# Optimization experiments

Hardware: AMD Instinct MI355X
Metric: run time of the kernel (lower is better)

The kernel has to match this reference:

```python
import jax, jax.numpy as jnp
import numpy as np

T, D, E, I = 2048, 2048, 16, 1408  # tokens, hidden, experts, moe intermediate


def setup_inputs() -> dict:
    key = jax.random.key(0)
    k1, k2, k3, k4 = jax.random.split(key, 4)
    return {
        "hidden_states": jax.random.normal(k1, (T, D), dtype=jnp.float32),
        "gate_w": jax.random.normal(k2, (E, D), dtype=jnp.float32) * 0.02,
        "w13": jax.random.normal(k3, (E, 2 * I, D), dtype=jnp.float32) * 0.02,
        "w2": jax.random.normal(k4, (E, D, I), dtype=jnp.float32) * 0.02,
        "top_k": 6,
    }


def reference(hidden_states, gate_w, w13, w2, top_k):
    x = hidden_states                               # [T, D]
    n_tokens, n_experts = x.shape[0], gate_w.shape[0]

    # Router gate + softmax + top-k (select_experts, use_grouped_topk=False)
    router_logits = x @ gate_w.T                    # [T, E]
    probs = jax.nn.softmax(router_logits, axis=-1)
    topk_w, topk_ids = jax.lax.top_k(probs, top_k)  # [T, K]
    # renormalize=True
    topk_w = topk_w / jnp.sum(topk_w, axis=-1, keepdims=True)

    # Dense combine weights [T, E]: scatter top-k weights to their experts
    combine = jnp.zeros((n_tokens, n_experts), dtype=x.dtype)
    combine = combine.at[jnp.arange(n_tokens)[:, None], topk_ids].add(topk_w)

    # Fused MoE experts: SwiGLU (w13 = fused gate+up), activation='silu'
    w1g = w13[:, : w13.shape[1] // 2, :]            # [E, I, D] gate proj
    w1u = w13[:, w13.shape[1] // 2 :, :]            # [E, I, D] up proj
    g = jnp.einsum("td,eid->tei", x, w1g)           # [T, E, I]
    u = jnp.einsum("td,eid->tei", x, w1u)
    h = jax.nn.silu(g) * u                          # [T, E, I]
    # Down proj + weighted combine over experts
    out = jnp.einsum("tei,edi,te->td", h, w2, combine)  # [T, D]
    return out
```

## Files before the change

### kernel.cpp

```cpp
#include <hip/hip_runtime.h>

#define T_TOK 2048
#define DIM 2048
#define NE 16
#define NI 1408
#define TOPK 6

typedef __bf16 bf16x8 __attribute__((ext_vector_type(8)));
typedef float f32x4 __attribute__((ext_vector_type(4)));

static __device__ __forceinline__ unsigned short f2bf(float f) {
  unsigned int u = __builtin_bit_cast(unsigned int, f);
  u += 0x7fffu + ((u >> 16) & 1u);
  return (unsigned short)(u >> 16);
}

static __device__ __forceinline__ void async_load16(const void* g, void* l) {
  __builtin_amdgcn_global_load_lds(
      (const __attribute__((address_space(1))) unsigned int*)g,
      (__attribute__((address_space(3))) unsigned int*)l, 16, 0, 0);
}

__global__ void router_kernel(const float* __restrict__ x, const float* __restrict__ gw,
                              float* __restrict__ combine) {
  int t = blockIdx.x;
  int l = threadIdx.x;
  const float* xr = x + (size_t)t * DIM;
  float acc[NE];
#pragma unroll
  for (int e = 0; e < NE; e++) acc[e] = 0.f;
  for (int d = l; d < DIM; d += 64) {
    float xv = xr[d];
#pragma unroll
    for (int e = 0; e < NE; e++) acc[e] += xv * gw[e * DIM + d];
  }
#pragma unroll
  for (int e = 0; e < NE; e++) {
    float v = acc[e];
#pragma unroll
    for (int s = 32; s > 0; s >>= 1) v += __shfl_down(v, s, 64);
    acc[e] = v;
  }
  if (l == 0) {
    float mx = acc[0];
#pragma unroll
    for (int e = 1; e < NE; e++) mx = fmaxf(mx, acc[e]);
    float p[NE]; float sum = 0.f;
#pragma unroll
    for (int e = 0; e < NE; e++) { p[e] = expf(acc[e] - mx); sum += p[e]; }
    float inv = 1.f / sum;
#pragma unroll
    for (int e = 0; e < NE; e++) p[e] *= inv;
    float w[NE];
#pragma unroll
    for (int e = 0; e < NE; e++) w[e] = 0.f;
    int used = 0;
    float ssum = 0.f;
    for (int k = 0; k < TOPK; k++) {
      int best = 0; float bv = -1e30f;
      for (int e = 0; e < NE; e++) {
        if (!((used >> e) & 1) && acc[e] > bv) { bv = acc[e]; best = e; }
      }
      used |= (1 << best);
      w[best] = p[best];
      ssum += p[best];
    }
    float isum = 1.f / ssum;
    for (int e = 0; e < NE; e++) combine[t * NE + e] = w[e] * isum;
  }
}

__global__ void cast_x_kernel(const float* __restrict__ x, unsigned short* __restrict__ xb) {
  int i = (blockIdx.x * 256 + threadIdx.x) * 4;
  float4 v = *(const float4*)(x + i);
  ushort4 o = make_ushort4(f2bf(v.x), f2bf(v.y), f2bf(v.z), f2bf(v.w));
  *(ushort4*)(xb + i) = o;
}

__global__ void count_kernel(const float* __restrict__ combine, int* __restrict__ counts) {
  int e = blockIdx.x, l = threadIdx.x;
  int c = 0;
  for (int t0 = 0; t0 < T_TOK; t0 += 64) {
    bool pred = combine[(size_t)(t0 + l) * NE + e] > 0.f;
    unsigned long long m = __ballot(pred);
    c += (int)__popcll(m);
  }
  if (l == 0) counts[e] = c;
}

__global__ void scan_kernel(const int* __restrict__ counts, int* __restrict__ offsets) {
  if (threadIdx.x == 0) {
    int s = 0;
    for (int e = 0; e < NE; e++) { offsets[e] = s; s += counts[e]; }
    offsets[NE] = s;
  }
}

__global__ void fill_kernel(const float* __restrict__ combine, const int* __restrict__ offsets,
                            int* __restrict__ ids, float* __restrict__ scales) {
  int e = blockIdx.x, l = threadIdx.x;
  int base = offsets[e];
  for (int t0 = 0; t0 < T_TOK; t0 += 64) {
    int t = t0 + l;
    float w = combine[(size_t)t * NE + e];
    bool pred = w > 0.f;
    unsigned long long m = __ballot(pred);
    int idx = base + (int)__popcll(m & ((1ull << l) - 1ull));
    if (pred) { ids[idx] = t; scales[idx] = w; }
    base += (int)__popcll(m);
  }
}

__global__ __launch_bounds__(256) void gemm1_kernel(
    const unsigned short* __restrict__ xb, const float* __restrict__ w13,
    const int* __restrict__ ids, const int* __restrict__ offsets,
    unsigned short* __restrict__ h) {
  int e = blockIdx.z;
  int off = offsets[e];
  int ne = offsets[e + 1] - off;
  int m0 = blockIdx.y * 128;
  if (m0 >= ne) return;
  int i0 = blockIdx.x * 64;

  __shared__ unsigned short At[8 * 128 * 8];
  __shared__ unsigned short Bg[8 * 64 * 8];
  __shared__ unsigned short Bu[8 * 64 * 8];
  __shared__ int ids_l[128];

  int tid = threadIdx.x;
  int wave = tid >> 6, lane = tid & 63;

  if (tid < 128) {
    int s = m0 + tid;
    ids_l[tid] = (s < ne) ? ids[off + s] : 0;
  }
  __syncthreads();
  int gid0 = ids_l[lane];
  int gid1 = ids_l[64 + lane];
  const unsigned short* a0 = xb + (size_t)gid0 * DIM;
  const unsigned short* a1 = xb + (size_t)gid1 * DIM;

  const float* We = w13 + (size_t)e * (2 * NI) * DIM;
  const float* Wg = We + (size_t)i0 * DIM;
  const float* Wu = We + (size_t)(NI + i0) * DIM;

  int wm = wave >> 1, wn = wave & 1;
  int quad = lane >> 4, l15 = lane & 15;

  f32x4 zf = {0.f, 0.f, 0.f, 0.f};
  f32x4 accg[4][2], accu[4][2];
#pragma unroll
  for (int a = 0; a < 4; a++)
#pragma unroll
    for (int b = 0; b < 2; b++) { accg[a][b] = zf; accu[a][b] = zf; }

  int brow = tid >> 4;
  int c4 = tid & 15;
  int bchunk = c4 >> 1;
  int hof = (c4 & 1) * 4;

  for (int k0 = 0; k0 < DIM; k0 += 64) {
#pragma unroll
    for (int j = 0; j < 4; j++) {
      int linear = wave * 4 + j;
      int chunk = linear >> 1;
      int half = j & 1;
      const unsigned short* src = (half ? a1 : a0) + k0 + chunk * 8;
      async_load16(src, &At[chunk * 1024 + half * 512]);
    }
#pragma unroll
    for (int r = 0; r < 4; r++) {
      int row = brow + r * 16;
      float4 vg = *(const float4*)(Wg + (size_t)row * DIM + k0 + c4 * 4);
      float4 vu = *(const float4*)(Wu + (size_t)row * DIM + k0 + c4 * 4);
      ushort4 og = make_ushort4(f2bf(vg.x), f2bf(vg.y), f2bf(vg.z), f2bf(vg.w));
      ushort4 ou = make_ushort4(f2bf(vu.x), f2bf(vu.y), f2bf(vu.z), f2bf(vu.w));
      *(ushort4*)&Bg[bchunk * 512 + row * 8 + hof] = og;
      *(ushort4*)&Bu[bchunk * 512 + row * 8 + hof] = ou;
    }
    __syncthreads();
#pragma unroll
    for (int ks = 0; ks < 2; ks++) {
      int cb = ks * 4 + quad;
      bf16x8 af[4], bgf[2], buf_[2];
#pragma unroll
      for (int mt = 0; mt < 4; mt++)
        af[mt] = *(const bf16x8*)&At[cb * 1024 + (wm * 64 + mt * 16 + l15) * 8];
#pragma unroll
      for (int nt = 0; nt < 2; nt++) {
        bgf[nt] = *(const bf16x8*)&Bg[cb * 512 + (wn * 32 + nt * 16 + l15) * 8];
        buf_[nt] = *(const bf16x8*)&Bu[cb * 512 + (wn * 32 + nt * 16 + l15) * 8];
      }
#pragma unroll
      for (int mt = 0; mt < 4; mt++)
#pragma unroll
        for (int nt = 0; nt < 2; nt++) {
          accg[mt][nt] = __builtin_amdgcn_mfma_f32_16x16x32_bf16(af[mt], bgf[nt], accg[mt][nt], 0, 0, 0);
          accu[mt][nt] = __builtin_amdgcn_mfma_f32_16x16x32_bf16(af[mt], buf_[nt], accu[mt][nt], 0, 0, 0);
        }
    }
    __syncthreads();
  }
#pragma unroll
  for (int mt = 0; mt < 4; mt++)
#pragma unroll
    for (int nt = 0; nt < 2; nt++)
#pragma unroll
      for (int r = 0; r < 4; r++) {
        int row_l = wm * 64 + mt * 16 + quad * 4 + r;
        if (m0 + row_l < ne) {
          float gv = accg[mt][nt][r];
          float uv = accu[mt][nt][r];
          float hv = gv * uv / (1.f + __expf(-gv));
          int col = i0 + wn * 32 + nt * 16 + l15;
          h[(size_t)(off + m0 + row_l) * NI + col] = f2bf(hv);
        }
      }
}

__global__ __launch_bounds__(256) void gemm2_kernel(
    const unsigned short* __restrict__ h, const float* __restrict__ w2,
    const int* __restrict__ ids, const float* __restrict__ scales,
    const int* __restrict__ offsets, float* __restrict__ out) {
  int e = blockIdx.z;
  int off = offsets[e];
  int ne = offsets[e + 1] - off;
  int m0 = blockIdx.y * 128;
  if (m0 >= ne) return;
  int n0 = blockIdx.x * 128;

  __shared__ unsigned short At[8 * 128 * 8];
  __shared__ unsigned short Bt[8 * 128 * 8];
  __shared__ int ids_l[128];
  __shared__ float scl_l[128];

  int tid = threadIdx.x;
  int wave = tid >> 6, lane = tid & 63;
  if (tid < 128) {
    int s = m0 + tid;
    bool v = s < ne;
    ids_l[tid] = v ? ids[off + s] : 0;
    scl_l[tid] = v ? scales[off + s] : 0.f;
  }
  __syncthreads();

  const unsigned short* h0 = h + (size_t)(off + m0 + lane) * NI;
  const unsigned short* h1 = h + (size_t)(off + m0 + 64 + lane) * NI;
  const float* W = w2 + (size_t)e * DIM * NI;

  int wm = wave >> 1, wn = wave & 1;
  int quad = lane >> 4, l15 = lane & 15;

  f32x4 zf = {0.f, 0.f, 0.f, 0.f};
  f32x4 acc[4][4];
#pragma unroll
  for (int a = 0; a < 4; a++)
#pragma unroll
    for (int b = 0; b < 4; b++) acc[a][b] = zf;

  int brow = tid >> 4, c4 = tid & 15, bchunk = c4 >> 1, hof = (c4 & 1) * 4;

  for (int k0 = 0; k0 < NI; k0 += 64) {
#pragma unroll
    for (int j = 0; j < 4; j++) {
      int linear = wave * 4 + j;
      int chunk = linear >> 1;
      int half = j & 1;
      const unsigned short* src = (half ? h1 : h0) + k0 + chunk * 8;
      async_load16(src, &At[chunk * 1024 + half * 512]);
    }
#pragma unroll
    for (int r = 0; r < 8; r++) {
      int row = brow + r * 16;
      float4 v = *(const float4*)(W + (size_t)(n0 + row) * NI + k0 + c4 * 4);
      ushort4 o = make_ushort4(f2bf(v.x), f2bf(v.y), f2bf(v.z), f2bf(v.w));
      *(ushort4*)&Bt[bchunk * 1024 + row * 8 + hof] = o;
    }
    __syncthreads();
#pragma unroll
    for (int ks = 0; ks < 2; ks++) {
      int cb = ks * 4 + quad;
      bf16x8 af[4], bf[4];
#pragma unroll
      for (int mt = 0; mt < 4; mt++)
        af[mt] = *(const bf16x8*)&At[cb * 1024 + (wm * 64 + mt * 16 + l15) * 8];
#pragma unroll
      for (int nt = 0; nt < 4; nt++)
        bf[nt] = *(const bf16x8*)&Bt[cb * 1024 + (wn * 64 + nt * 16 + l15) * 8];
#pragma unroll
      for (int mt = 0; mt < 4; mt++)
#pragma unroll
        for (int nt = 0; nt < 4; nt++)
          acc[mt][nt] = __builtin_amdgcn_mfma_f32_16x16x32_bf16(af[mt], bf[nt], acc[mt][nt], 0, 0, 0);
    }
    __syncthreads();
  }
#pragma unroll
  for (int mt = 0; mt < 4; mt++)
#pragma unroll
    for (int nt = 0; nt < 4; nt++)
#pragma unroll
      for (int r = 0; r < 4; r++) {
        int row_l = wm * 64 + mt * 16 + quad * 4 + r;
        if (m0 + row_l < ne) {
          int t = ids_l[row_l];
          float s = scl_l[row_l];
          int col = n0 + wn * 64 + nt * 16 + l15;
          atomicAdd(&out[(size_t)t * DIM + col], s * acc[mt][nt][r]);
        }
      }
}

extern "C" void kernel_launch(void* const* d_in, const int* in_sizes, int n_in,
                              void* d_out, int out_size, void* d_ws, size_t ws_size,
                              hipStream_t stream) {
  const float* x   = (const float*)d_in[0];
  const float* gw  = (const float*)d_in[1];
  const float* w13 = (const float*)d_in[2];
  const float* w2  = (const float*)d_in[3];
  float* out = (float*)d_out;

  char* ws = (char*)d_ws;
  float* combine        = (float*)(ws + 0x000000);
  int* counts           = (int*)  (ws + 0x020000);
  int* offsets          = (int*)  (ws + 0x020100);
  int* ids              = (int*)  (ws + 0x020200);
  float* scales         = (float*)(ws + 0x02D000);
  unsigned short* xb    = (unsigned short*)(ws + 0x040000);
  unsigned short* h     = (unsigned short*)(ws + 0x840000);

  hipMemsetAsync(d_out, 0, (size_t)T_TOK * DIM * sizeof(float), stream);

  router_kernel<<<T_TOK, 64, 0, stream>>>(x, gw, combine);
  cast_x_kernel<<<(T_TOK * DIM) / (256 * 4), 256, 0, stream>>>(x, xb);
  count_kernel<<<NE, 64, 0, stream>>>(combine, counts);
  scan_kernel<<<1, 64, 0, stream>>>(counts, offsets);
  fill_kernel<<<NE, 64, 0, stream>>>(combine, offsets, ids, scales);

  gemm1_kernel<<<dim3(NI / 64, T_TOK / 128, NE), 256, 0, stream>>>(xb, w13, ids, offsets, h);
  gemm2_kernel<<<dim3(DIM / 128, T_TOK / 128, NE), 256, 0, stream>>>(h, w2, ids, scales, offsets, out);
}
```

Measured before the change: 1.201 ms.

## Pre-cast expert weights to bf16 in chunks before grouped GEMMs

Adds a weight-cast kernel that converts chunks of w13 and w2 from fp32 to bf16 in workspace, then runs new GEMM kernels that load bf16 weights directly with async LDS loads. The old kernels re-read fp32 weights and converted them in each tile, so the same weights were fetched and converted once per token block. The new path adds an extra full pass over the weights and more kernel launches per chunk. It needs enough workspace, and falls back to the old kernels when there is not enough.

```diff
diff --git a/kernel.cpp b/kernel.cpp
--- a/kernel.cpp
+++ b/kernel.cpp
@@ -75,6 +75,16 @@
   float4 v = *(const float4*)(x + i);
   ushort4 o = make_ushort4(f2bf(v.x), f2bf(v.y), f2bf(v.z), f2bf(v.w));
   *(ushort4*)(xb + i) = o;
+}
+
+__global__ void cast_w_kernel(const float* __restrict__ src, unsigned short* __restrict__ dst,
+                              int n4) {
+  int stride = gridDim.x * 256;
+  for (int i = blockIdx.x * 256 + threadIdx.x; i < n4; i += stride) {
+    float4 v = ((const float4*)src)[i];
+    ushort4 o = make_ushort4(f2bf(v.x), f2bf(v.y), f2bf(v.z), f2bf(v.w));
+    ((ushort4*)dst)[i] = o;
+  }
 }
 
 __global__ void count_kernel(const float* __restrict__ combine, int* __restrict__ counts) {
@@ -111,7 +121,188 @@
   }
 }
 
-__global__ __launch_bounds__(256) void gemm1_kernel(
+
+__global__ __launch_bounds__(256) void gemm1_pre_kernel(
+    const unsigned short* __restrict__ xb, const unsigned short* __restrict__ wb,
+    const int* __restrict__ ids, const int* __restrict__ offsets,
+    unsigned short* __restrict__ h, int e_base) {
+  int ez = blockIdx.z;
+  int e = e_base + ez;
+  int off = offsets[e];
+  int ne = offsets[e + 1] - off;
+  int m0 = blockIdx.y * 128;
+  if (m0 >= ne) return;
+  int i0 = blockIdx.x * 64;
+
+  __shared__ unsigned short At[8 * 128 * 8];
+  __shared__ unsigned short Bg[8 * 64 * 8];
+  __shared__ unsigned short Bu[8 * 64 * 8];
+  __shared__ int ids_l[128];
+
+  int tid = threadIdx.x;
+  int wave = tid >> 6, lane = tid & 63;
+
+  if (tid < 128) {
+    int s = m0 + tid;
+    ids_l[tid] = (s < ne) ? ids[off + s] : 0;
+  }
+  __syncthreads();
+  const unsigned short* a0 = xb + (size_t)ids_l[lane] * DIM;
+  const unsigned short* a1 = xb + (size_t)ids_l[64 + lane] * DIM;
+  const unsigned short* wg = wb + ((size_t)ez * (2 * NI) + i0 + lane) * DIM;
+  const unsigned short* wu = wb + ((size_t)ez * (2 * NI) + NI + i0 + lane) * DIM;
+
+  int wm = wave >> 1, wn = wave & 1;
+  int quad = lane >> 4, l15 = lane & 15;
+
+  f32x4 zf = {0.f, 0.f, 0.f, 0.f};
+  f32x4 accg[4][2], accu[4][2];
+#pragma unroll
+  for (int a = 0; a < 4; a++)
+#pragma unroll
+    for (int b = 0; b < 2; b++) { accg[a][b] = zf; accu[a][b] = zf; }
+
+  for (int k0 = 0; k0 < DIM; k0 += 64) {
+#pragma unroll
+    for (int j = 0; j < 4; j++) {
+      int linear = wave * 4 + j;
+      int c = linear >> 1;
+      int half = j & 1;
+      async_load16((half ? a1 : a0) + k0 + c * 8, &At[c * 1024 + half * 512]);
+    }
+#pragma unroll
+    for (int j = 0; j < 2; j++) {
+      int c = wave * 2 + j;
+      async_load16(wg + k0 + c * 8, &Bg[c * 512]);
+      async_load16(wu + k0 + c * 8, &Bu[c * 512]);
+    }
+    __syncthreads();
+#pragma unroll
+    for (int ks = 0; ks < 2; ks++) {
+      int cb = ks * 4 + quad;
+      bf16x8 af[4], bgf[2], buf_[2];
+#pragma unroll
+      for (int mt = 0; mt < 4; mt++)
+        af[mt] = *(const bf16x8*)&At[cb * 1024 + (wm * 64 + mt * 16 + l15) * 8];
+#pragma unroll
+      for (int nt = 0; nt < 2; nt++) {
+        bgf[nt] = *(const bf16x8*)&Bg[cb * 512 + (wn * 32 + nt * 16 + l15) * 8];
+        buf_[nt] = *(const bf16x8*)&Bu[cb * 512 + (wn * 32 + nt * 16 + l15) * 8];
+      }
+#pragma unroll
+      for (int mt = 0; mt < 4; mt++)
+#pragma unroll
+        for (int nt = 0; nt < 2; nt++) {
+          accg[mt][nt] = __builtin_amdgcn_mfma_f32_16x16x32_bf16(af[mt], bgf[nt], accg[mt][nt], 0, 0, 0);
+          accu[mt][nt] = __builtin_amdgcn_mfma_f32_16x16x32_bf16(af[mt], buf_[nt], accu[mt][nt], 0, 0, 0);
+        }
+    }
+    __syncthreads();
+  }
+#pragma unroll
+  for (int mt = 0; mt < 4; mt++)
+#pragma unroll
+    for (int nt = 0; nt < 2; nt++)
+#pragma unroll
+      for (int r = 0; r < 4; r++) {
+        int row_l = wm * 64 + mt * 16 + quad * 4 + r;
+        if (m0 + row_l < ne) {
+          float gv = accg[mt][nt][r];
+          float uv = accu[mt][nt][r];
+          float hv = gv * uv / (1.f + __expf(-gv));
+          int col = i0 + wn * 32 + nt * 16 + l15;
+          h[(size_t)(off + m0 + row_l) * NI + col] = f2bf(hv);
+        }
+      }
+}
+
+__global__ __launch_bounds__(256) void gemm2_pre_kernel(
+    const unsigned short* __restrict__ h, const unsigned short* __restrict__ wb,
+    const int* __restrict__ ids, const float* __restrict__ scales,
+    const int* __restrict__ offsets, float* __restrict__ out, int e_base) {
+  int ez = blockIdx.z;
+  int e = e_base + ez;
+  int off = offsets[e];
+  int ne = offsets[e + 1] - off;
+  int m0 = blockIdx.y * 128;
+  if (m0 >= ne) return;
+  int n0 = blockIdx.x * 128;
+
+  __shared__ unsigned short At[8 * 128 * 8];
+  __shared__ unsigned short Bt[8 * 128 * 8];
+  __shared__ int ids_l[128];
+  __shared__ float scl_l[128];
+
+  int tid = threadIdx.x;
+  int wave = tid >> 6, lane = tid & 63;
+  if (tid < 128) {
+    int s = m0 + tid;
+    bool v = s < ne;
+    ids_l[tid] = v ? ids[off + s] : 0;
+    scl_l[tid] = v ? scales[off + s] : 0.f;
+  }
+  __syncthreads();
+
+  const unsigned short* h0 = h + (size_t)(off + m0 + lane) * NI;
+  const unsigned short* h1 = h + (size_t)(off + m0 + 64 + lane) * NI;
+  const unsigned short* b0 = wb + ((size_t)ez * DIM + n0 + lane) * NI;
+  const unsigned short* b1 = b0 + (size_t)64 * NI;
+
+  int wm = wave >> 1, wn = wave & 1;
+  int quad = lane >> 4, l15 = lane & 15;
+
+  f32x4 zf = {0.f, 0.f, 0.f, 0.f};
+  f32x4 acc[4][4];
+#pragma unroll
+  for (int a = 0; a < 4; a++)
+#pragma unroll
+    for (int b = 0; b < 4; b++) acc[a][b] = zf;
+
+  for (int k0 = 0; k0 < NI; k0 += 64) {
+#pragma unroll
+    for (int j = 0; j < 4; j++) {
+      int linear = wave * 4 + j;
+      int c = linear >> 1;
+      int half = j & 1;
+      async_load16((half ? h1 : h0) + k0 + c * 8, &At[c * 1024 + half * 512]);
+      async_load16((half ? b1 : b0) + k0 + c * 8, &Bt[c * 1024 + half * 512]);
+    }
+    __syncthreads();
+#pragma unroll
+    for (int ks = 0; ks < 2; ks++) {
+      int cb = ks * 4 + quad;
+      bf16x8 af[4], bf[4];
+#pragma unroll
+      for (int mt = 0; mt < 4; mt++)
+        af[mt] = *(const bf16x8*)&At[cb * 1024 + (wm * 64 + mt * 16 + l15) * 8];
+#pragma unroll
+      for (int nt = 0; nt < 4; nt++)
+        bf[nt] = *(const bf16x8*)&Bt[cb * 1024 + (wn * 64 + nt * 16 + l15) * 8];
+#pragma unroll
+      for (int mt = 0; mt < 4; mt++)
+#pragma unroll
+        for (int nt = 0; nt < 4; nt++)
+          acc[mt][nt] = __builtin_amdgcn_mfma_f32_16x16x32_bf16(af[mt], bf[nt], acc[mt][nt], 0, 0, 0);
+    }
+    __syncthreads();
+  }
+#pragma unroll
+  for (int mt = 0; mt < 4; mt++)
+#pragma unroll
+    for (int nt = 0; nt < 4; nt++)
+#pragma unroll
+      for (int r = 0; r < 4; r++) {
+        int row_l = wm * 64 + mt * 16 + quad * 4 + r;
+        if (m0 + row_l < ne) {
+          int t = ids_l[row_l];
+          float s = scl_l[row_l];
+          int col = n0 + wn * 64 + nt * 16 + l15;
+          atomicAdd(&out[(size_t)t * DIM + col], s * acc[mt][nt][r]);
+        }
+      }
+}
+
+__global__ __launch_bounds__(256) void gemm1_fb_kernel(
     const unsigned short* __restrict__ xb, const float* __restrict__ w13,
     const int* __restrict__ ids, const int* __restrict__ offsets,
     unsigned short* __restrict__ h) {
@@ -218,7 +409,7 @@
       }
 }
 
-__global__ __launch_bounds__(256) void gemm2_kernel(
+__global__ __launch_bounds__(256) void gemm2_fb_kernel(
     const unsigned short* __restrict__ h, const float* __restrict__ w2,
     const int* __restrict__ ids, const float* __restrict__ scales,
     const int* __restrict__ offsets, float* __restrict__ out) {
@@ -328,6 +519,14 @@
   float* scales         = (float*)(ws + 0x02D000);
   unsigned short* xb    = (unsigned short*)(ws + 0x040000);
   unsigned short* h     = (unsigned short*)(ws + 0x840000);
+  unsigned short* wb    = (unsigned short*)(ws + 0x2A00000);
+
+  const size_t wb_off = 0x2A00000;
+  const size_t per_e13 = (size_t)(2 * NI) * DIM * 2;
+  int chunk = 0;
+  if      (ws_size >= wb_off + 8 * per_e13) chunk = 8;
+  else if (ws_size >= wb_off + 4 * per_e13) chunk = 4;
+  else if (ws_size >= wb_off + 2 * per_e13) chunk = 2;
 
   hipMemsetAsync(d_out, 0, (size_t)T_TOK * DIM * sizeof(float), stream);
 
@@ -337,6 +536,21 @@
   scan_kernel<<<1, 64, 0, stream>>>(counts, offsets);
   fill_kernel<<<NE, 64, 0, stream>>>(combine, offsets, ids, scales);
 
-  gemm1_kernel<<<dim3(NI / 64, T_TOK / 128, NE), 256, 0, stream>>>(xb, w13, ids, offsets, h);
-  gemm2_kernel<<<dim3(DIM / 128, T_TOK / 128, NE), 256, 0, stream>>>(h, w2, ids, scales, offsets, out);
-}
+  if (chunk) {
+    for (int b = 0; b < NE; b += chunk) {
+      int n4 = chunk * 2 * NI * DIM / 4;
+      cast_w_kernel<<<2048, 256, 0, stream>>>(w13 + (size_t)b * (2 * NI) * DIM, wb, n4);
+      gemm1_pre_kernel<<<dim3(NI / 64, T_TOK / 128, chunk), 256, 0, stream>>>(
+          xb, wb, ids, offsets, h, b);
+    }
+    for (int b = 0; b < NE; b += chunk) {
+      int n4 = chunk * DIM * NI / 4;
+      cast_w_kernel<<<2048, 256, 0, stream>>>(w2 + (size_t)b * DIM * NI, wb, n4);
+      gemm2_pre_kernel<<<dim3(DIM / 128, T_TOK / 128, chunk), 256, 0, stream>>>(
+          h, wb, ids, scales, offsets, out, b);
+    }
+  } else {
+    gemm1_fb_kernel<<<dim3(NI / 64, T_TOK / 128, NE), 256, 0, stream>>>(xb, w13, ids, offsets, h);
+    gemm2_fb_kernel<<<dim3(DIM / 128, T_TOK / 128, NE), 256, 0, stream>>>(h, w2, ids, scales, offsets, out);
+  }
+}
```

New measurement: 1.326 ms. +10.5%, slower.

## Double-buffer LDS tiles, swizzle B layout, and remap grid for XCD locality

Applied to the files above, without the earlier changes.

Both expert GEMM kernels now double-buffer the A and B shared-memory tiles. The next tile's async A loads and global B loads are issued before the current tile's MFMAs, which drops one barrier per k-step and overlaps memory with compute. The B tile is written with an XOR swizzle to reduce LDS bank conflicts, and the 3D grid is flattened into a 1D grid with an interleaved block-to-tile mapping across the 8 XCDs. In exchange, shared memory per block doubles and register pressure rises from holding prefetched B values, which may lower occupancy.

```diff
diff --git a/kernel.cpp b/kernel.cpp
--- a/kernel.cpp
+++ b/kernel.cpp
@@ -115,16 +115,21 @@
     const unsigned short* __restrict__ xb, const float* __restrict__ w13,
     const int* __restrict__ ids, const int* __restrict__ offsets,
     unsigned short* __restrict__ h) {
-  int e = blockIdx.z;
+  int bid = blockIdx.x;
+  int lin = (bid & 7) * (5632 >> 3) + (bid >> 3);
+  int iy = lin & 15;
+  int ix = (lin >> 4) % 22;
+  int e  = lin / 352;
+
   int off = offsets[e];
   int ne = offsets[e + 1] - off;
-  int m0 = blockIdx.y * 128;
+  int m0 = iy * 128;
   if (m0 >= ne) return;
-  int i0 = blockIdx.x * 64;
-
-  __shared__ unsigned short At[8 * 128 * 8];
-  __shared__ unsigned short Bg[8 * 64 * 8];
-  __shared__ unsigned short Bu[8 * 64 * 8];
+  int i0 = ix * 64;
+
+  __shared__ unsigned short At[2][8 * 128 * 8];
+  __shared__ unsigned short Bg[2][8 * 64 * 8];
+  __shared__ unsigned short Bu[2][8 * 64 * 8];
   __shared__ int ids_l[128];
 
   int tid = threadIdx.x;
@@ -135,10 +140,8 @@
     ids_l[tid] = (s < ne) ? ids[off + s] : 0;
   }
   __syncthreads();
-  int gid0 = ids_l[lane];
-  int gid1 = ids_l[64 + lane];
-  const unsigned short* a0 = xb + (size_t)gid0 * DIM;
-  const unsigned short* a1 = xb + (size_t)gid1 * DIM;
+  const unsigned short* a0 = xb + (size_t)ids_l[lane] * DIM;
+  const unsigned short* a1 = xb + (size_t)ids_l[64 + lane] * DIM;
 
   const float* We = w13 + (size_t)e * (2 * NI) * DIM;
   const float* Wg = We + (size_t)i0 * DIM;
@@ -147,60 +150,85 @@
   int wm = wave >> 1, wn = wave & 1;
   int quad = lane >> 4, l15 = lane & 15;
 
-  f32x4 zf = {0.f, 0.f, 0.f, 0.f};
-  f32x4 accg[4][2], accu[4][2];
-#pragma unroll
-  for (int a = 0; a < 4; a++)
-#pragma unroll
-    for (int b = 0; b < 2; b++) { accg[a][b] = zf; accu[a][b] = zf; }
-
   int brow = tid >> 4;
   int c4 = tid & 15;
   int bchunk = c4 >> 1;
-  int hof = (c4 & 1) * 4;
-
-  for (int k0 = 0; k0 < DIM; k0 += 64) {
-#pragma unroll
-    for (int j = 0; j < 4; j++) {
-      int linear = wave * 4 + j;
-      int chunk = linear >> 1;
-      int half = j & 1;
-      const unsigned short* src = (half ? a1 : a0) + k0 + chunk * 8;
-      async_load16(src, &At[chunk * 1024 + half * 512]);
-    }
-#pragma unroll
-    for (int r = 0; r < 4; r++) {
-      int row = brow + r * 16;
-      float4 vg = *(const float4*)(Wg + (size_t)row * DIM + k0 + c4 * 4);
-      float4 vu = *(const float4*)(Wu + (size_t)row * DIM + k0 + c4 * 4);
-      ushort4 og = make_ushort4(f2bf(vg.x), f2bf(vg.y), f2bf(vg.z), f2bf(vg.w));
-      ushort4 ou = make_ushort4(f2bf(vu.x), f2bf(vu.y), f2bf(vu.z), f2bf(vu.w));
-      *(ushort4*)&Bg[bchunk * 512 + row * 8 + hof] = og;
-      *(ushort4*)&Bu[bchunk * 512 + row * 8 + hof] = ou;
-    }
+  int hof2 = (c4 & 1) * 8;
+
+  f32x4 zf = {0.f, 0.f, 0.f, 0.f};
+  f32x4 accg[4][2], accu[4][2];
+#pragma unroll
+  for (int a = 0; a < 4; a++)
+#pragma unroll
+    for (int b = 0; b < 2; b++) { accg[a][b] = zf; accu[a][b] = zf; }
+
+#define G1_STAGE_A(P, K0)                                                      \
+  _Pragma("unroll") for (int j = 0; j < 4; j++) {                              \
+    int c = (wave * 4 + j) >> 1;                                               \
+    int half = j & 1;                                                          \
+    async_load16((half ? a1 : a0) + (K0) + c * 8, &At[P][c * 1024 + half * 512]); \
+  }
+
+#define G1_LOAD_B(K0)                                                          \
+  _Pragma("unroll") for (int r = 0; r < 4; r++) {                              \
+    int row = brow + r * 16;                                                   \
+    vg[r] = *(const float4*)(Wg + (size_t)row * DIM + (K0) + c4 * 4);          \
+    vu[r] = *(const float4*)(Wu + (size_t)row * DIM + (K0) + c4 * 4);          \
+  }
+
+#define G1_WRITE_B(P)                                                          \
+  _Pragma("unroll") for (int r = 0; r < 4; r++) {                              \
+    int row = brow + r * 16;                                                   \
+    int swz = (bchunk * 1024 + row * 16 + hof2) ^ (bchunk << 4);               \
+    ushort4 og = make_ushort4(f2bf(vg[r].x), f2bf(vg[r].y), f2bf(vg[r].z), f2bf(vg[r].w)); \
+    ushort4 ou = make_ushort4(f2bf(vu[r].x), f2bf(vu[r].y), f2bf(vu[r].z), f2bf(vu[r].w)); \
+    *(ushort4*)((char*)&Bg[P][0] + swz) = og;                                  \
+    *(ushort4*)((char*)&Bu[P][0] + swz) = ou;                                  \
+  }
+
+#define G1_COMPUTE(P)                                                          \
+  _Pragma("unroll") for (int ks = 0; ks < 2; ks++) {                           \
+    int cb = ks * 4 + quad;                                                    \
+    int cbx = cb << 4;                                                         \
+    bf16x8 af[4], bgf[2], buf_[2];                                             \
+    const char* Ab = (const char*)&At[P][0];                                   \
+    const char* Bgb = (const char*)&Bg[P][0];                                  \
+    const char* Bub = (const char*)&Bu[P][0];                                  \
+    _Pragma("unroll") for (int mt = 0; mt < 4; mt++)                           \
+      af[mt] = *(const bf16x8*)(Ab + cb * 2048 + (wm * 64 + mt * 16 + l15) * 16); \
+    _Pragma("unroll") for (int nt = 0; nt < 2; nt++) {                         \
+      int rb = cb * 1024 + (wn * 32 + nt * 16 + l15) * 16;                     \
+      bgf[nt] = *(const bf16x8*)(Bgb + (rb ^ cbx));                            \
+      buf_[nt] = *(const bf16x8*)(Bub + (rb ^ cbx));                           \
+    }                                                                          \
+    _Pragma("unroll") for (int mt = 0; mt < 4; mt++)                           \
+      _Pragma("unroll") for (int nt = 0; nt < 2; nt++) {                       \
+        accg[mt][nt] = __builtin_amdgcn_mfma_f32_16x16x32_bf16(af[mt], bgf[nt], accg[mt][nt], 0, 0, 0); \
+        accu[mt][nt] = __builtin_amdgcn_mfma_f32_16x16x32_bf16(af[mt], buf_[nt], accu[mt][nt], 0, 0, 0); \
+      }                                                                        \
+  }
+
+  {
+    float4 vg[4], vu[4];
+    G1_STAGE_A(0, 0)
+    G1_LOAD_B(0)
+    G1_WRITE_B(0)
+  }
+  __syncthreads();
+
+  int p = 0;
+  for (int t = 0; t < DIM / 64 - 1; t++) {
+    int k1 = (t + 1) * 64;
+    float4 vg[4], vu[4];
+    G1_STAGE_A(p ^ 1, k1)
+    G1_LOAD_B(k1)
+    G1_COMPUTE(p)
+    G1_WRITE_B(p ^ 1)
     __syncthreads();
-#pragma unroll
-    for (int ks = 0; ks < 2; ks++) {
-      int cb = ks * 4 + quad;
-      bf16x8 af[4], bgf[2], buf_[2];
-#pragma unroll
-      for (int mt = 0; mt < 4; mt++)
-        af[mt] = *(const bf16x8*)&At[cb * 1024 + (wm * 64 + mt * 16 + l15) * 8];
-#pragma unroll
-      for (int nt = 0; nt < 2; nt++) {
-        bgf[nt] = *(const bf16x8*)&Bg[cb * 512 + (wn * 32 + nt * 16 + l15) * 8];
-        buf_[nt] = *(const bf16x8*)&Bu[cb * 512 + (wn * 32 + nt * 16 + l15) * 8];
-      }
-#pragma unroll
-      for (int mt = 0; mt < 4; mt++)
-#pragma unroll
-        for (int nt = 0; nt < 2; nt++) {
-          accg[mt][nt] = __builtin_amdgcn_mfma_f32_16x16x32_bf16(af[mt], bgf[nt], accg[mt][nt], 0, 0, 0);
-          accu[mt][nt] = __builtin_amdgcn_mfma_f32_16x16x32_bf16(af[mt], buf_[nt], accu[mt][nt], 0, 0, 0);
-        }
-    }
-    __syncthreads();
-  }
+    p ^= 1;
+  }
+  G1_COMPUTE(p)
+
 #pragma unroll
   for (int mt = 0; mt < 4; mt++)
 #pragma unroll
@@ -216,21 +244,30 @@
           h[(size_t)(off + m0 + row_l) * NI + col] = f2bf(hv);
         }
       }
+#undef G1_STAGE_A
+#undef G1_LOAD_B
+#undef G1_WRITE_B
+#undef G1_COMPUTE
 }
 
 __global__ __launch_bounds__(256) void gemm2_kernel(
     const unsigned short* __restrict__ h, const float* __restrict__ w2,
     const int* __restrict__ ids, const float* __restrict__ scales,
     const int* __restrict__ offsets, float* __restrict__ out) {
-  int e = blockIdx.z;
+  int bid = blockIdx.x;
+  int lin = (bid & 7) * (4096 >> 3) + (bid >> 3);
+  int iy = lin & 15;
+  int ix = (lin >> 4) & 15;
+  int e  = lin >> 8;
+
   int off = offsets[e];
   int ne = offsets[e + 1] - off;
-  int m0 = blockIdx.y * 128;
+  int m0 = iy * 128;
   if (m0 >= ne) return;
-  int n0 = blockIdx.x * 128;
-
-  __shared__ unsigned short At[8 * 128 * 8];
-  __shared__ unsigned short Bt[8 * 128 * 8];
+  int n0 = ix * 128;
+
+  __shared__ unsigned short At[2][8 * 128 * 8];
+  __shared__ unsigned short Bt[2][8 * 128 * 8];
   __shared__ int ids_l[128];
   __shared__ float scl_l[128];
 
@@ -246,11 +283,16 @@
 
   const unsigned short* h0 = h + (size_t)(off + m0 + lane) * NI;
   const unsigned short* h1 = h + (size_t)(off + m0 + 64 + lane) * NI;
-  const float* W = w2 + (size_t)e * DIM * NI;
+  const float* W = w2 + (size_t)e * DIM * NI + (size_t)n0 * NI;
 
   int wm = wave >> 1, wn = wave & 1;
   int quad = lane >> 4, l15 = lane & 15;
 
+  int brow = tid >> 4;
+  int c4 = tid & 15;
+  int bchunk = c4 >> 1;
+  int hof2 = (c4 & 1) * 8;
+
   f32x4 zf = {0.f, 0.f, 0.f, 0.f};
   f32x4 acc[4][4];
 #pragma unroll
@@ -258,43 +300,66 @@
 #pragma unroll
     for (int b = 0; b < 4; b++) acc[a][b] = zf;
 
-  int brow = tid >> 4, c4 = tid & 15, bchunk = c4 >> 1, hof = (c4 & 1) * 4;
-
-  for (int k0 = 0; k0 < NI; k0 += 64) {
-#pragma unroll
-    for (int j = 0; j < 4; j++) {
-      int linear = wave * 4 + j;
-      int chunk = linear >> 1;
-      int half = j & 1;
-      const unsigned short* src = (half ? h1 : h0) + k0 + chunk * 8;
-      async_load16(src, &At[chunk * 1024 + half * 512]);
-    }
-#pragma unroll
-    for (int r = 0; r < 8; r++) {
-      int row = brow + r * 16;
-      float4 v = *(const float4*)(W + (size_t)(n0 + row) * NI + k0 + c4 * 4);
-      ushort4 o = make_ushort4(f2bf(v.x), f2bf(v.y), f2bf(v.z), f2bf(v.w));
-      *(ushort4*)&Bt[bchunk * 1024 + row * 8 + hof] = o;
-    }
+#define G2_STAGE_A(P, K0)                                                      \
+  _Pragma("unroll") for (int j = 0; j < 4; j++) {                              \
+    int c = (wave * 4 + j) >> 1;                                               \
+    int half = j & 1;                                                          \
+    async_load16((half ? h1 : h0) + (K0) + c * 8, &At[P][c * 1024 + half * 512]); \
+  }
+
+#define G2_LOAD_B(K0)                                                          \
+  _Pragma("unroll") for (int r = 0; r < 8; r++) {                              \
+    int row = brow + r * 16;                                                   \
+    vb[r] = *(const float4*)(W + (size_t)row * NI + (K0) + c4 * 4);            \
+  }
+
+#define G2_WRITE_B(P)                                                          \
+  _Pragma("unroll") for (int r = 0; r < 8; r++) {                              \
+    int row = brow + r * 16;                                                   \
+    int swz = (bchunk * 2048 + row * 16 + hof2) ^ (bchunk << 4);               \
+    ushort4 o = make_ushort4(f2bf(vb[r].x), f2bf(vb[r].y), f2bf(vb[r].z), f2bf(vb[r].w)); \
+    *(ushort4*)((char*)&Bt[P][0] + swz) = o;                                   \
+  }
+
+#define G2_COMPUTE(P)                                                          \
+  _Pragma("unroll") for (int ks = 0; ks < 2; ks++) {                           \
+    int cb = ks * 4 + quad;                                                    \
+    int cbx = cb << 4;                                                         \
+    bf16x8 af[4], bf[4];                                                       \
+    const char* Ab = (const char*)&At[P][0];                                   \
+    const char* Bb = (const char*)&Bt[P][0];                                   \
+    _Pragma("unroll") for (int mt = 0; mt < 4; mt++)                           \
+      af[mt] = *(const bf16x8*)(Ab + cb * 2048 + (wm * 64 + mt * 16 + l15) * 16); \
+    _Pragma("unroll") for (int nt = 0; nt < 4; nt++) {                         \
+      int rb = cb * 2048 + (wn * 64 + nt * 16 + l15) * 16;                     \
+      bf[nt] = *(const bf16x8*)(Bb + (rb ^ cbx));                              \
+    }                                                                          \
+    _Pragma("unroll") for (int mt = 0; mt < 4; mt++)                           \
+      _Pragma("unroll") for (int nt = 0; nt < 4; nt++)                         \
+        acc[mt][nt] = __builtin_amdgcn_mfma_f32_16x16x32_bf16(af[mt], bf[nt], acc[mt][nt], 0, 0, 0); \
+  }
+
+  {
+    float4 vb[8];
+    G2_STAGE_A(0, 0)
+    G2_LOAD_B(0)
+    G2_WRITE_B(0)
+  }
+  __syncthreads();
+
+  int p = 0;
+  for (int t = 0; t < NI / 64 - 1; t++) {
+    int k1 = (t + 1) * 64;
+    float4 vb[8];
+    G2_STAGE_A(p ^ 1, k1)
+    G2_LOAD_B(k1)
+    G2_COMPUTE(p)
+    G2_WRITE_B(p ^ 1)
     __syncthreads();
-#pragma unroll
-    for (int ks = 0; ks < 2; ks++) {
-      int cb = ks * 4 + quad;
-      bf16x8 af[4], bf[4];
-#pragma unroll
-      for (int mt = 0; mt < 4; mt++)
-        af[mt] = *(const bf16x8*)&At[cb * 1024 + (wm * 64 + mt * 16 + l15) * 8];
-#pragma unroll
-      for (int nt = 0; nt < 4; nt++)
-        bf[nt] = *(const bf16x8*)&Bt[cb * 1024 + (wn * 64 + nt * 16 + l15) * 8];
-#pragma unroll
-      for (int mt = 0; mt < 4; mt++)
-#pragma unroll
-        for (int nt = 0; nt < 4; nt++)
-          acc[mt][nt] = __builtin_amdgcn_mfma_f32_16x16x32_bf16(af[mt], bf[nt], acc[mt][nt], 0, 0, 0);
-    }
-    __syncthreads();
-  }
+    p ^= 1;
+  }
+  G2_COMPUTE(p)
+
 #pragma unroll
   for (int mt = 0; mt < 4; mt++)
 #pragma unroll
@@ -309,6 +374,10 @@
           atomicAdd(&out[(size_t)t * DIM + col], s * acc[mt][nt][r]);
         }
       }
+#undef G2_STAGE_A
+#undef G2_LOAD_B
+#undef G2_WRITE_B
+#undef G2_COMPUTE
 }
 
 extern "C" void kernel_launch(void* const* d_in, const int* in_sizes, int n_in,
@@ -337,6 +406,6 @@
   scan_kernel<<<1, 64, 0, stream>>>(counts, offsets);
   fill_kernel<<<NE, 64, 0, stream>>>(combine, offsets, ids, scales);
 
-  gemm1_kernel<<<dim3(NI / 64, T_TOK / 128, NE), 256, 0, stream>>>(xb, w13, ids, offsets, h);
-  gemm2_kernel<<<dim3(DIM / 128, T_TOK / 128, NE), 256, 0, stream>>>(h, w2, ids, scales, offsets, out);
-}
+  gemm1_kernel<<<16 * 22 * 16, 256, 0, stream>>>(xb, w13, ids, offsets, h);
+  gemm2_kernel<<<16 * 16 * 16, 256, 0, stream>>>(h, w2, ids, scales, offsets, out);
+}
```

Measured after the change: 1.199 ms. Within noise of the previous version (-0.1%).
